# Optimization experiments

Hardware: AMD Instinct MI355X
Metric: run time of the kernel (lower is better)

## Reference

```python
import jax, jax.numpy as jnp
import numpy as np

N = 50000
E = 1600000
IN_F = 256
OUT_F = 128
ALPHA = 0.2  # LeakyReLU negative slope


def setup_inputs() -> dict:
    key = jax.random.key(0)
    k1, k2, k3, k4, k5, k6 = jax.random.split(key, 6)
    h = jax.random.normal(k1, (N, IN_F), dtype=jnp.float32)
    src = jax.random.randint(k2, (E,), 0, N, dtype=jnp.int64)
    dst = jax.random.randint(k3, (E,), 0, N, dtype=jnp.int64)
    # xavier_uniform-style init
    def xavier(k, shape):
        bound = np.sqrt(6.0 / (shape[0] + shape[1]))
        return jax.random.uniform(k, shape, jnp.float32, -bound, bound)
    W = xavier(k4, (IN_F, OUT_F))
    a_src = xavier(k5, (OUT_F, 1))
    a_dst = xavier(k6, (OUT_F, 1))
    return {"h": h, "src": src, "dst": dst, "W": W, "a_src": a_src, "a_dst": a_dst}


def reference(h, src, dst, W, a_src, a_dst):
    n = h.shape[0]
    Wh = h @ W                                  # [N, OUT_F] dense GEMM
    f1 = (Wh @ a_src)[:, 0]                     # [N]
    f2 = (Wh @ a_dst)[:, 0]                     # [N]
    e = f1[src] + f2[dst]                       # [E] edge-wise gather
    e = jnp.where(e > 0, e, ALPHA * e)          # LeakyReLU
    # sparse softmax over each row (segment = src/row index)
    m = jax.ops.segment_max(e, src, num_segments=n)
    ex = jnp.exp(e - m[src])
    denom = jax.ops.segment_sum(ex, src, num_segments=n)
    att = ex / denom[src]                       # [E] normalized attention
    # sparse-dense matmul: h_prime[i] = sum_j att[ij] * Wh[j]
    h_prime = jax.ops.segment_sum(att[:, None] * Wh[dst], src, num_segments=n)
    return jax.nn.elu(h_prime)
```

## Files before the change

### kernel.cpp

```cpp
#include <hip/hip_runtime.h>
#include <hip/hip_bf16.h>
#include <math.h>

#define IN_F 256
#define OUT_F 128
#define ALPHA 0.2f

#define BSH 7
#define BNODES 128
#define CHUNK 8192
#define NBK 512
#define CAP 5120

typedef __attribute__((ext_vector_type(8))) short short8;
typedef __attribute__((ext_vector_type(4))) float f32x4;
typedef __attribute__((ext_vector_type(2))) float f32x2;

static __device__ __forceinline__ unsigned short f2bf(float x) {
    union { __hip_bfloat16 h; unsigned short u; } cv;
    cv.h = __float2bfloat16(x);
    return cv.u;
}

static __device__ __forceinline__ f32x2 up2(unsigned int u) {
    union { float f; unsigned int i; } lo, hi;
    lo.i = u << 16;
    hi.i = u & 0xFFFF0000u;
    return (f32x2){lo.f, hi.f};
}

__global__ __launch_bounds__(512) void scatter_gemm_kernel(
        const int* __restrict__ src, const int* __restrict__ dst,
        int* __restrict__ cursor, unsigned int* __restrict__ bin, int e, int nb,
        const float* __restrict__ h, const float* __restrict__ W,
        const float* __restrict__ a_src, const float* __restrict__ a_dst,
        unsigned short* __restrict__ Whb, float* __restrict__ f1,
        float* __restrict__ f2, int n, int nsc) {
    __shared__ union {
        struct {
            unsigned int ebuf[CHUNK];
            int lh[NBK];
            int ls[NBK];
            int ebase[NBK];
            int lx[NBK];
            int gbase[NBK];
        } sc;
        struct {
            unsigned short a[128 * 40];
            unsigned short b[128 * 40];
        } ge;
    } sm;
    int tid = threadIdx.x;

    if ((int)blockIdx.x < nsc) {
        int base = blockIdx.x * CHUNK;
        int count = e - base; if (count > CHUNK) count = CHUNK;

        for (int i = tid; i < nb; i += 512) sm.sc.lh[i] = 0;
        __syncthreads();
        for (int i = tid; i < count; i += 512) atomicAdd(&sm.sc.lh[src[base + i] >> BSH], 1);
        __syncthreads();
        int v = (tid < nb) ? sm.sc.lh[tid] : 0;
        sm.sc.ls[tid] = v;
        __syncthreads();
#pragma unroll
        for (int off = 1; off < NBK; off <<= 1) {
            int t = (tid >= off) ? sm.sc.ls[tid - off] : 0;
            __syncthreads();
            sm.sc.ls[tid] += t;
            __syncthreads();
        }
        if (tid < nb) {
            int ex = sm.sc.ls[tid] - v;
            sm.sc.ebase[tid] = ex;
            sm.sc.lx[tid] = ex;
        }
        __syncthreads();
        for (int i = tid; i < count; i += 512) {
            int s = src[base + i], d = dst[base + i];
            int b = s >> BSH;
            int p = atomicAdd(&sm.sc.lx[b], 1);
            sm.sc.ebuf[p] = ((unsigned int)(s & (BNODES - 1)) << 17) | (unsigned int)d;
        }
        __syncthreads();
        if (tid < nb) {
            int c = sm.sc.lh[tid];
            sm.sc.gbase[tid] = c ? atomicAdd(&cursor[tid], c) : 0;
        }
        __syncthreads();
        int wave = tid >> 6, lane = tid & 63;
        for (int b = wave; b < nb; b += 8) {
            int c = sm.sc.lh[b], eb = sm.sc.ebase[b], gb = sm.sc.gbase[b];
            size_t gb0 = (size_t)b * CAP + gb;
            for (int l = lane; l < c; l += 64) bin[gb0 + l] = sm.sc.ebuf[eb + l];
        }
    } else {
        int bid = blockIdx.x - nsc;
        int wv = tid >> 6, lane = tid & 63;
        int m = lane & 15, quad = lane >> 4;
        int r0 = bid * 128;

        f32x4 acc[8];
#pragma unroll
        for (int c = 0; c < 8; c++) acc[c] = (f32x4){0.f, 0.f, 0.f, 0.f};

        int bcol = tid & 127;
        int bkq  = tid >> 7;

        for (int k0 = 0; k0 < IN_F; k0 += 32) {
            {
                int arow = tid >> 3;
                int kq = tid & 7;
#pragma unroll
                for (int p = 0; p < 2; p++) {
                    int row = arow + p * 64;
                    int grow = r0 + row;
                    float4 v = make_float4(0.f, 0.f, 0.f, 0.f);
                    if (grow < n) v = *(const float4*)&h[(size_t)grow * IN_F + k0 + kq * 4];
                    ushort4 b;
                    b.x = f2bf(v.x); b.y = f2bf(v.y); b.z = f2bf(v.z); b.w = f2bf(v.w);
                    *(ushort4*)&sm.ge.a[row * 40 + kq * 4] = b;
                }
            }
            {
                float vw[8];
#pragma unroll
                for (int j = 0; j < 8; ++j)
                    vw[j] = W[(size_t)(k0 + bkq * 8 + j) * OUT_F + bcol];
                union { short8 v; unsigned short u[8]; } pk;
#pragma unroll
                for (int j = 0; j < 8; ++j) pk.u[j] = f2bf(vw[j]);
                *(short8*)&sm.ge.b[bcol * 40 + bkq * 8] = pk.v;
            }
            __syncthreads();
            short8 af = *(const short8*)&sm.ge.a[(wv * 16 + m) * 40 + quad * 8];
#pragma unroll
            for (int c = 0; c < 8; c++) {
                short8 bfv = *(const short8*)&sm.ge.b[(c * 16 + m) * 40 + quad * 8];
                acc[c] = __builtin_amdgcn_mfma_f32_16x16x32_bf16(af, bfv, acc[c], 0, 0, 0);
            }
            __syncthreads();
        }

        int base_row = r0 + wv * 16 + quad * 4;
#pragma unroll
        for (int reg = 0; reg < 4; reg++) {
            int rg = base_row + reg;
            if (rg < n) {
#pragma unroll
                for (int c = 0; c < 8; c++)
                    Whb[(size_t)rg * OUT_F + c * 16 + m] = f2bf(acc[c][reg]);
            }
        }

        float a1[8], a2[8];
#pragma unroll
        for (int c = 0; c < 8; c++) {
            a1[c] = a_src[c * 16 + m];
            a2[c] = a_dst[c * 16 + m];
        }
        float p1[4] = {0.f, 0.f, 0.f, 0.f}, p2[4] = {0.f, 0.f, 0.f, 0.f};
#pragma unroll
        for (int c = 0; c < 8; c++)
#pragma unroll
            for (int reg = 0; reg < 4; reg++) {
                p1[reg] += acc[c][reg] * a1[c];
                p2[reg] += acc[c][reg] * a2[c];
            }
#pragma unroll
        for (int mask = 1; mask < 16; mask <<= 1)
#pragma unroll
            for (int reg = 0; reg < 4; reg++) {
                p1[reg] += __shfl_xor(p1[reg], mask, 64);
                p2[reg] += __shfl_xor(p2[reg], mask, 64);
            }
        if (m == 0) {
#pragma unroll
            for (int reg = 0; reg < 4; reg++) {
                int rg = base_row + reg;
                if (rg < n) { f1[rg] = p1[reg]; f2[rg] = p2[reg]; }
            }
        }
    }
}

__global__ __launch_bounds__(512) void sortagg_kernel(
        const int* __restrict__ cursor, const unsigned int* __restrict__ bin,
        const float* __restrict__ f1, const float* __restrict__ f2,
        const unsigned int* __restrict__ WhbU, float* __restrict__ out, int n) {
    __shared__ uint2 eL[CAP];
    __shared__ int lh[BNODES];
    __shared__ int st[BNODES];
    __shared__ int cur[BNODES];
    __shared__ int scn[BNODES];
    __shared__ float lf1[BNODES];
    int b = blockIdx.x;
    int tid = threadIdx.x;
    int base = b * CAP;
    int K = cursor[b];
    if (K > CAP) K = CAP;

    if (tid < BNODES) {
        lh[tid] = 0;
        int node = (b << BSH) + tid;
        lf1[tid] = (node < n) ? f1[node] : 0.f;
    }
    __syncthreads();

    unsigned int pe[10];
#pragma unroll
    for (int u = 0; u < 10; ++u) {
        int i = tid + u * 512;
        if (i < K) {
            unsigned int p = bin[base + i];
            pe[u] = p;
            atomicAdd(&lh[p >> 17], 1);
        }
    }
    __syncthreads();

    if (tid < BNODES) {
        int lane = tid & 63;
        int s = lh[tid];
#pragma unroll
        for (int off = 1; off < 64; off <<= 1) {
            int t = __shfl_up(s, off, 64);
            if (lane >= off) s += t;
        }
        scn[tid] = s;
    }
    __syncthreads();
    if (tid < BNODES) {
        int inc = scn[tid] + ((tid >= 64) ? scn[63] : 0);
        int start = inc - lh[tid];
        st[tid] = start;
        cur[tid] = start;
    }
    __syncthreads();

#pragma unroll
    for (int u = 0; u < 10; ++u) {
        int i = tid + u * 512;
        if (i < K) {
            unsigned int p = pe[u];
            int ls_ = p >> 17;
            int d = p & 0x1FFFF;
            int r = atomicAdd(&cur[ls_], 1);
            float e = lf1[ls_] + f2[d];
            e = e > 0.f ? e : ALPHA * e;
            eL[r] = make_uint2((unsigned int)d, __float_as_uint(__expf(e)));
        }
    }
    __syncthreads();

    int wv = tid >> 6, lane = tid & 63;
    int grp = lane >> 4, c8 = lane & 15;
    for (int li = 0; li < 16; ++li) {
        int l = (wv << 4) + li;
        int node = (b << BSH) + l;
        int dg = lh[l];
        int j = st[l];
        int jend = j + dg;
        f32x2 a0 = {0.f, 0.f}, a1 = {0.f, 0.f}, a2 = {0.f, 0.f}, a3 = {0.f, 0.f};
        float den = 0.f;
        for (; j + 16 <= jend; j += 16) {
            uint2 e0 = eL[j + grp];
            uint2 e1 = eL[j + grp + 4];
            uint2 e2 = eL[j + grp + 8];
            uint2 e3 = eL[j + grp + 12];
            uint4 w0 = *(const uint4*)&WhbU[((size_t)e0.x << 6) + (c8 << 2)];
            uint4 w1 = *(const uint4*)&WhbU[((size_t)e1.x << 6) + (c8 << 2)];
            uint4 w2 = *(const uint4*)&WhbU[((size_t)e2.x << 6) + (c8 << 2)];
            uint4 w3 = *(const uint4*)&WhbU[((size_t)e3.x << 6) + (c8 << 2)];
            float x0 = __uint_as_float(e0.y);
            float x1 = __uint_as_float(e1.y);
            float x2 = __uint_as_float(e2.y);
            float x3 = __uint_as_float(e3.y);
            f32x2 xx;
            xx = (f32x2){x0, x0};
            a0 += xx * up2(w0.x); a1 += xx * up2(w0.y); a2 += xx * up2(w0.z); a3 += xx * up2(w0.w);
            xx = (f32x2){x1, x1};
            a0 += xx * up2(w1.x); a1 += xx * up2(w1.y); a2 += xx * up2(w1.z); a3 += xx * up2(w1.w);
            xx = (f32x2){x2, x2};
            a0 += xx * up2(w2.x); a1 += xx * up2(w2.y); a2 += xx * up2(w2.z); a3 += xx * up2(w2.w);
            xx = (f32x2){x3, x3};
            a0 += xx * up2(w3.x); a1 += xx * up2(w3.y); a2 += xx * up2(w3.z); a3 += xx * up2(w3.w);
            den += x0 + x1 + x2 + x3;
        }
        for (; j + 4 <= jend; j += 4) {
            uint2 e = eL[j + grp];
            uint4 w = *(const uint4*)&WhbU[((size_t)e.x << 6) + (c8 << 2)];
            float x = __uint_as_float(e.y);
            f32x2 xx = {x, x};
            a0 += xx * up2(w.x); a1 += xx * up2(w.y); a2 += xx * up2(w.z); a3 += xx * up2(w.w);
            den += x;
        }
        if (j + grp < jend) {
            uint2 e = eL[j + grp];
            uint4 w = *(const uint4*)&WhbU[((size_t)e.x << 6) + (c8 << 2)];
            float x = __uint_as_float(e.y);
            f32x2 xx = {x, x};
            a0 += xx * up2(w.x); a1 += xx * up2(w.y); a2 += xx * up2(w.z); a3 += xx * up2(w.w);
            den += x;
        }

#pragma unroll
        for (int mask = 16; mask < 64; mask <<= 1) {
            a0.x += __shfl_xor(a0.x, mask, 64);
            a0.y += __shfl_xor(a0.y, mask, 64);
            a1.x += __shfl_xor(a1.x, mask, 64);
            a1.y += __shfl_xor(a1.y, mask, 64);
            a2.x += __shfl_xor(a2.x, mask, 64);
            a2.y += __shfl_xor(a2.y, mask, 64);
            a3.x += __shfl_xor(a3.x, mask, 64);
            a3.y += __shfl_xor(a3.y, mask, 64);
            den += __shfl_xor(den, mask, 64);
        }

        if (grp == 0 && node < n) {
            float inv = dg ? 1.f / den : 0.f;
            float r[8];
            r[0] = a0.x * inv; r[1] = a0.y * inv; r[2] = a1.x * inv; r[3] = a1.y * inv;
            r[4] = a2.x * inv; r[5] = a2.y * inv; r[6] = a3.x * inv; r[7] = a3.y * inv;
#pragma unroll
            for (int k = 0; k < 8; k++) r[k] = r[k] > 0.f ? r[k] : __expf(r[k]) - 1.f;
            float* op = &out[(size_t)node * OUT_F + c8 * 8];
            *(float4*)&op[0] = make_float4(r[0], r[1], r[2], r[3]);
            *(float4*)&op[4] = make_float4(r[4], r[5], r[6], r[7]);
        }
    }
}

extern "C" void kernel_launch(void* const* d_in, const int* in_sizes, int n_in,
                              void* d_out, int out_size, void* d_ws, size_t ws_size,
                              hipStream_t stream) {
    const float* h     = (const float*)d_in[0];
    const int*   src   = (const int*)d_in[1];
    const int*   dst   = (const int*)d_in[2];
    const float* W     = (const float*)d_in[3];
    const float* a_src = (const float*)d_in[4];
    const float* a_dst = (const float*)d_in[5];
    float* out = (float*)d_out;

    const int N = in_sizes[0] / IN_F;
    const int E = in_sizes[1];
    const int NB = (N + BNODES - 1) >> BSH;
    const int NCH = (E + CHUNK - 1) / CHUNK;
    const int GB = (N + 127) / 128;

    char* ws = (char*)d_ws;
    size_t off = 0;
    auto alloc = [&](size_t bytes) -> void* {
        void* p = ws + off;
        off += (bytes + 255) & ~(size_t)255;
        return p;
    };
    unsigned short* Whb = (unsigned short*)alloc((size_t)N * OUT_F * 2);
    float* f1     = (float*)alloc((size_t)N * 4);
    float* f2     = (float*)alloc((size_t)N * 4);
    int*   cursor = (int*)alloc((size_t)NB * 4);
    unsigned int* bin = (unsigned int*)alloc((size_t)NB * CAP * 4);
    (void)ws_size; (void)n_in; (void)out_size;

    hipMemsetAsync(cursor, 0, (size_t)NB * 4, stream);
    scatter_gemm_kernel<<<NCH + GB, 512, 0, stream>>>(src, dst, cursor, bin, E, NB,
                                                      h, W, a_src, a_dst, Whb, f1, f2, N, NCH);
    sortagg_kernel<<<NB, 512, 0, stream>>>(cursor, bin, f1, f2,
                                           (const unsigned int*)Whb, out, N);
}
```

Measured before the change: 189.5 us.

## Split each aggregation bucket across two blocks of 64 nodes

```diff
diff --git a/kernel.cpp b/kernel.cpp
--- a/kernel.cpp
+++ b/kernel.cpp
@@ -11,6 +11,8 @@
 #define CHUNK 8192
 #define NBK 512
 #define CAP 5120
+#define HNODES 64
+#define HCAP 3072
 
 typedef __attribute__((ext_vector_type(8))) short short8;
 typedef __attribute__((ext_vector_type(4))) float f32x4;
@@ -188,21 +190,22 @@
         const int* __restrict__ cursor, const unsigned int* __restrict__ bin,
         const float* __restrict__ f1, const float* __restrict__ f2,
         const unsigned int* __restrict__ WhbU, float* __restrict__ out, int n) {
-    __shared__ uint2 eL[CAP];
-    __shared__ int lh[BNODES];
-    __shared__ int st[BNODES];
-    __shared__ int cur[BNODES];
-    __shared__ int scn[BNODES];
-    __shared__ float lf1[BNODES];
-    int b = blockIdx.x;
+    __shared__ uint2 eL[HCAP];
+    __shared__ int lh[HNODES];
+    __shared__ int st[HNODES];
+    __shared__ int cur[HNODES];
+    __shared__ float lf1[HNODES];
+    int b = blockIdx.x >> 1;
+    int half = blockIdx.x & 1;
     int tid = threadIdx.x;
     int base = b * CAP;
+    int node0 = (b << BSH) + half * HNODES;
     int K = cursor[b];
     if (K > CAP) K = CAP;
 
-    if (tid < BNODES) {
+    if (tid < HNODES) {
         lh[tid] = 0;
-        int node = (b << BSH) + tid;
+        int node = node0 + tid;
         lf1[tid] = (node < n) ? f1[node] : 0.f;
     }
     __syncthreads();
@@ -210,29 +213,28 @@
     unsigned int pe[10];
 #pragma unroll
     for (int u = 0; u < 10; ++u) {
+        unsigned int p = 0xFFFFFFFFu;
         int i = tid + u * 512;
         if (i < K) {
-            unsigned int p = bin[base + i];
-            pe[u] = p;
-            atomicAdd(&lh[p >> 17], 1);
-        }
+            unsigned int q = bin[base + i];
+            int ls = q >> 17;
+            if ((ls >> 6) == half) {
+                p = q;
+                atomicAdd(&lh[ls & (HNODES - 1)], 1);
+            }
+        }
+        pe[u] = p;
     }
     __syncthreads();
 
-    if (tid < BNODES) {
-        int lane = tid & 63;
+    if (tid < HNODES) {
         int s = lh[tid];
 #pragma unroll
         for (int off = 1; off < 64; off <<= 1) {
             int t = __shfl_up(s, off, 64);
-            if (lane >= off) s += t;
-        }
-        scn[tid] = s;
-    }
-    __syncthreads();
-    if (tid < BNODES) {
-        int inc = scn[tid] + ((tid >= 64) ? scn[63] : 0);
-        int start = inc - lh[tid];
+            if (tid >= off) s += t;
+        }
+        int start = s - lh[tid];
         st[tid] = start;
         cur[tid] = start;
     }
@@ -240,24 +242,23 @@
 
 #pragma unroll
     for (int u = 0; u < 10; ++u) {
-        int i = tid + u * 512;
-        if (i < K) {
-            unsigned int p = pe[u];
-            int ls_ = p >> 17;
+        unsigned int p = pe[u];
+        if (p != 0xFFFFFFFFu) {
+            int ls_ = (p >> 17) & (HNODES - 1);
             int d = p & 0x1FFFF;
             int r = atomicAdd(&cur[ls_], 1);
             float e = lf1[ls_] + f2[d];
             e = e > 0.f ? e : ALPHA * e;
-            eL[r] = make_uint2((unsigned int)d, __float_as_uint(__expf(e)));
+            if (r < HCAP) eL[r] = make_uint2((unsigned int)d, __float_as_uint(__expf(e)));
         }
     }
     __syncthreads();
 
     int wv = tid >> 6, lane = tid & 63;
     int grp = lane >> 4, c8 = lane & 15;
-    for (int li = 0; li < 16; ++li) {
-        int l = (wv << 4) + li;
-        int node = (b << BSH) + l;
+    for (int li = 0; li < 8; ++li) {
+        int l = (wv << 3) + li;
+        int node = node0 + l;
         int dg = lh[l];
         int j = st[l];
         int jend = j + dg;
@@ -365,6 +366,6 @@
     hipMemsetAsync(cursor, 0, (size_t)NB * 4, stream);
     scatter_gemm_kernel<<<NCH + GB, 512, 0, stream>>>(src, dst, cursor, bin, E, NB,
                                                       h, W, a_src, a_dst, Whb, f1, f2, N, NCH);
-    sortagg_kernel<<<NB, 512, 0, stream>>>(cursor, bin, f1, f2,
-                                           (const unsigned int*)Whb, out, N);
-}
+    sortagg_kernel<<<NB * 2, 512, 0, stream>>>(cursor, bin, f1, f2,
+                                               (const unsigned int*)Whb, out, N);
+}
```

After: 193.9 us. 1.02x slower.

## Split sort and aggregation; partition feature columns by XCC for L2 locality

Applied to the files above, without the earlier changes.

```diff
diff --git a/kernel.cpp b/kernel.cpp
--- a/kernel.cpp
+++ b/kernel.cpp
@@ -184,16 +184,18 @@
     }
 }
 
-__global__ __launch_bounds__(512) void sortagg_kernel(
+__global__ __launch_bounds__(512) void sort_kernel(
         const int* __restrict__ cursor, const unsigned int* __restrict__ bin,
         const float* __restrict__ f1, const float* __restrict__ f2,
-        const unsigned int* __restrict__ WhbU, float* __restrict__ out, int n) {
+        uint2* __restrict__ edat, int* __restrict__ offs, int* __restrict__ deg,
+        float* __restrict__ inv, int n) {
     __shared__ uint2 eL[CAP];
     __shared__ int lh[BNODES];
     __shared__ int st[BNODES];
     __shared__ int cur[BNODES];
     __shared__ int scn[BNODES];
     __shared__ float lf1[BNODES];
+    __shared__ float lden[BNODES];
     int b = blockIdx.x;
     int tid = threadIdx.x;
     int base = b * CAP;
@@ -202,6 +204,7 @@
 
     if (tid < BNODES) {
         lh[tid] = 0;
+        lden[tid] = 0.f;
         int node = (b << BSH) + tid;
         lf1[tid] = (node < n) ? f1[node] : 0.f;
     }
@@ -231,8 +234,8 @@
     }
     __syncthreads();
     if (tid < BNODES) {
-        int inc = scn[tid] + ((tid >= 64) ? scn[63] : 0);
-        int start = inc - lh[tid];
+        int incl = scn[tid] + ((tid >= 64) ? scn[63] : 0);
+        int start = incl - lh[tid];
         st[tid] = start;
         cur[tid] = start;
     }
@@ -248,85 +251,101 @@
             int r = atomicAdd(&cur[ls_], 1);
             float e = lf1[ls_] + f2[d];
             e = e > 0.f ? e : ALPHA * e;
-            eL[r] = make_uint2((unsigned int)d, __float_as_uint(__expf(e)));
-        }
-    }
-    __syncthreads();
-
+            float ex = __expf(e);
+            atomicAdd(&lden[ls_], ex);
+            eL[r] = make_uint2((unsigned int)d, __float_as_uint(ex));
+        }
+    }
+    __syncthreads();
+
+    if (tid < BNODES) {
+        int node = (b << BSH) + tid;
+        if (node < n) {
+            offs[node] = base + st[tid];
+            deg[node] = lh[tid];
+            inv[node] = lh[tid] ? 1.f / lden[tid] : 0.f;
+        }
+    }
+    for (int i = tid; i < K; i += 512) edat[base + i] = eL[i];
+}
+
+__global__ __launch_bounds__(256) void aggq_kernel(
+        const int* __restrict__ cursor, const uint2* __restrict__ edat,
+        const int* __restrict__ offs, const int* __restrict__ deg,
+        const float* __restrict__ inv, const unsigned int* __restrict__ WhbU,
+        float* __restrict__ out, int* __restrict__ qcur, int n, int nb) {
+    __shared__ uint2 eL[CAP];
+    __shared__ float linv[BNODES];
+    __shared__ int lst[BNODES];
+    __shared__ int ldg[BNODES];
+    __shared__ int sb;
+    int tid = threadIdx.x;
+    unsigned int xcc;
+    asm("s_getreg_b32 %0, hwreg(HW_REG_XCC_ID)" : "=s"(xcc));
+    int q = xcc & 3;
     int wv = tid >> 6, lane = tid & 63;
-    int grp = lane >> 4, c8 = lane & 15;
-    for (int li = 0; li < 16; ++li) {
-        int l = (wv << 4) + li;
-        int node = (b << BSH) + l;
-        int dg = lh[l];
-        int j = st[l];
-        int jend = j + dg;
-        f32x2 a0 = {0.f, 0.f}, a1 = {0.f, 0.f}, a2 = {0.f, 0.f}, a3 = {0.f, 0.f};
-        float den = 0.f;
-        for (; j + 16 <= jend; j += 16) {
-            uint2 e0 = eL[j + grp];
-            uint2 e1 = eL[j + grp + 4];
-            uint2 e2 = eL[j + grp + 8];
-            uint2 e3 = eL[j + grp + 12];
-            uint4 w0 = *(const uint4*)&WhbU[((size_t)e0.x << 6) + (c8 << 2)];
-            uint4 w1 = *(const uint4*)&WhbU[((size_t)e1.x << 6) + (c8 << 2)];
-            uint4 w2 = *(const uint4*)&WhbU[((size_t)e2.x << 6) + (c8 << 2)];
-            uint4 w3 = *(const uint4*)&WhbU[((size_t)e3.x << 6) + (c8 << 2)];
-            float x0 = __uint_as_float(e0.y);
-            float x1 = __uint_as_float(e1.y);
-            float x2 = __uint_as_float(e2.y);
-            float x3 = __uint_as_float(e3.y);
-            f32x2 xx;
-            xx = (f32x2){x0, x0};
-            a0 += xx * up2(w0.x); a1 += xx * up2(w0.y); a2 += xx * up2(w0.z); a3 += xx * up2(w0.w);
-            xx = (f32x2){x1, x1};
-            a0 += xx * up2(w1.x); a1 += xx * up2(w1.y); a2 += xx * up2(w1.z); a3 += xx * up2(w1.w);
-            xx = (f32x2){x2, x2};
-            a0 += xx * up2(w2.x); a1 += xx * up2(w2.y); a2 += xx * up2(w2.z); a3 += xx * up2(w2.w);
-            xx = (f32x2){x3, x3};
-            a0 += xx * up2(w3.x); a1 += xx * up2(w3.y); a2 += xx * up2(w3.z); a3 += xx * up2(w3.w);
-            den += x0 + x1 + x2 + x3;
-        }
-        for (; j + 4 <= jend; j += 4) {
-            uint2 e = eL[j + grp];
-            uint4 w = *(const uint4*)&WhbU[((size_t)e.x << 6) + (c8 << 2)];
-            float x = __uint_as_float(e.y);
-            f32x2 xx = {x, x};
-            a0 += xx * up2(w.x); a1 += xx * up2(w.y); a2 += xx * up2(w.z); a3 += xx * up2(w.w);
-            den += x;
-        }
-        if (j + grp < jend) {
-            uint2 e = eL[j + grp];
-            uint4 w = *(const uint4*)&WhbU[((size_t)e.x << 6) + (c8 << 2)];
-            float x = __uint_as_float(e.y);
-            f32x2 xx = {x, x};
-            a0 += xx * up2(w.x); a1 += xx * up2(w.y); a2 += xx * up2(w.z); a3 += xx * up2(w.w);
-            den += x;
-        }
-
-#pragma unroll
-        for (int mask = 16; mask < 64; mask <<= 1) {
-            a0.x += __shfl_xor(a0.x, mask, 64);
-            a0.y += __shfl_xor(a0.y, mask, 64);
-            a1.x += __shfl_xor(a1.x, mask, 64);
-            a1.y += __shfl_xor(a1.y, mask, 64);
-            a2.x += __shfl_xor(a2.x, mask, 64);
-            a2.y += __shfl_xor(a2.y, mask, 64);
-            a3.x += __shfl_xor(a3.x, mask, 64);
-            a3.y += __shfl_xor(a3.y, mask, 64);
-            den += __shfl_xor(den, mask, 64);
-        }
-
-        if (grp == 0 && node < n) {
-            float inv = dg ? 1.f / den : 0.f;
-            float r[8];
-            r[0] = a0.x * inv; r[1] = a0.y * inv; r[2] = a1.x * inv; r[3] = a1.y * inv;
-            r[4] = a2.x * inv; r[5] = a2.y * inv; r[6] = a3.x * inv; r[7] = a3.y * inv;
-#pragma unroll
-            for (int k = 0; k < 8; k++) r[k] = r[k] > 0.f ? r[k] : __expf(r[k]) - 1.f;
-            float* op = &out[(size_t)node * OUT_F + c8 * 8];
-            *(float4*)&op[0] = make_float4(r[0], r[1], r[2], r[3]);
-            *(float4*)&op[4] = make_float4(r[4], r[5], r[6], r[7]);
+    int e16 = lane >> 2, c = lane & 3;
+    int qtry = 0;
+
+    for (;;) {
+        __syncthreads();
+        if (tid == 0) sb = atomicAdd(&qcur[q], 1);
+        __syncthreads();
+        int b = sb;
+        if (b >= nb) {
+            q = (q + 1) & 3;
+            if (++qtry >= 4) break;
+            continue;
+        }
+        qtry = 0;
+        int base = b * CAP;
+        int K = cursor[b];
+        if (K > CAP) K = CAP;
+        if (tid < BNODES) {
+            int node = (b << BSH) + tid;
+            bool v = node < n;
+            lst[tid] = v ? (offs[node] - base) : 0;
+            ldg[tid] = v ? deg[node] : 0;
+            linv[tid] = v ? inv[node] : 0.f;
+        }
+        for (int i = tid; i < K; i += 256) eL[i] = edat[base + i];
+        __syncthreads();
+
+        const unsigned int* wq = WhbU + (q << 4) + (c << 2);
+        for (int l = wv; l < BNODES; l += 4) {
+            int dg = ldg[l];
+            int j0 = lst[l];
+            int jend = j0 + dg;
+            f32x2 a0 = {0.f, 0.f}, a1 = {0.f, 0.f}, a2 = {0.f, 0.f}, a3 = {0.f, 0.f};
+            int T = (dg + 15) >> 4;
+            for (int t = 0; t < T; ++t) {
+                int j = j0 + (t << 4) + e16;
+                uint2 e = eL[j < jend ? j : j0];
+                float x = (j < jend) ? __uint_as_float(e.y) : 0.f;
+                uint4 w = *(const uint4*)&wq[(size_t)e.x << 6];
+                f32x2 xx = {x, x};
+                a0 += xx * up2(w.x); a1 += xx * up2(w.y);
+                a2 += xx * up2(w.z); a3 += xx * up2(w.w);
+            }
+#pragma unroll
+            for (int mask = 4; mask < 64; mask <<= 1) {
+                a0.x += __shfl_xor(a0.x, mask, 64); a0.y += __shfl_xor(a0.y, mask, 64);
+                a1.x += __shfl_xor(a1.x, mask, 64); a1.y += __shfl_xor(a1.y, mask, 64);
+                a2.x += __shfl_xor(a2.x, mask, 64); a2.y += __shfl_xor(a2.y, mask, 64);
+                a3.x += __shfl_xor(a3.x, mask, 64); a3.y += __shfl_xor(a3.y, mask, 64);
+            }
+            int node = (b << BSH) + l;
+            if (e16 == 0 && node < n) {
+                float iv = linv[l];
+                float r[8];
+                r[0] = a0.x * iv; r[1] = a0.y * iv; r[2] = a1.x * iv; r[3] = a1.y * iv;
+                r[4] = a2.x * iv; r[5] = a2.y * iv; r[6] = a3.x * iv; r[7] = a3.y * iv;
+#pragma unroll
+                for (int k = 0; k < 8; ++k) r[k] = r[k] > 0.f ? r[k] : __expf(r[k]) - 1.f;
+                float* op = &out[(size_t)node * OUT_F + (q << 5) + (c << 3)];
+                *(float4*)&op[0] = make_float4(r[0], r[1], r[2], r[3]);
+                *(float4*)&op[4] = make_float4(r[4], r[5], r[6], r[7]);
+            }
         }
     }
 }
@@ -358,13 +377,19 @@
     unsigned short* Whb = (unsigned short*)alloc((size_t)N * OUT_F * 2);
     float* f1     = (float*)alloc((size_t)N * 4);
     float* f2     = (float*)alloc((size_t)N * 4);
-    int*   cursor = (int*)alloc((size_t)NB * 4);
-    unsigned int* bin = (unsigned int*)alloc((size_t)NB * CAP * 4);
+    int*   cursor = (int*)alloc((size_t)(NB + 8) * 4);
+    int*   offs   = (int*)alloc((size_t)N * 4);
+    int*   deg    = (int*)alloc((size_t)N * 4);
+    float* inv    = (float*)alloc((size_t)N * 4);
+    unsigned int* bin  = (unsigned int*)alloc((size_t)NB * CAP * 4);
+    uint2*        edat = (uint2*)alloc((size_t)NB * CAP * 8);
+    int* qcur = cursor + NB;
     (void)ws_size; (void)n_in; (void)out_size;
 
-    hipMemsetAsync(cursor, 0, (size_t)NB * 4, stream);
+    hipMemsetAsync(cursor, 0, (size_t)(NB + 8) * 4, stream);
     scatter_gemm_kernel<<<NCH + GB, 512, 0, stream>>>(src, dst, cursor, bin, E, NB,
                                                       h, W, a_src, a_dst, Whb, f1, f2, N, NCH);
-    sortagg_kernel<<<NB, 512, 0, stream>>>(cursor, bin, f1, f2,
-                                           (const unsigned int*)Whb, out, N);
-}
+    sort_kernel<<<NB, 512, 0, stream>>>(cursor, bin, f1, f2, edat, offs, deg, inv, N);
+    aggq_kernel<<<1024, 256, 0, stream>>>(cursor, edat, offs, deg, inv,
+                                          (const unsigned int*)Whb, out, qcur, N, NB);
+}
```

After: 341.3 us. 1.8x slower.
